# Kernel tuning notes

Hardware: AMD Instinct MI355X
Metric: run time of the kernel (lower is better)

## Reference

```python
import jax, jax.numpy as jnp
import numpy as np


def setup_inputs() -> dict:
    key = jax.random.key(0)
    k1, k2 = jax.random.split(key)
    inputs = jax.random.normal(k1, (64, 32, 32, 64), dtype=jnp.float32)
    # codebook param: (embedding_dim=64, n_embedding=1024), variance-scaling uniform fan_in
    fan_in = 64
    limit = float(np.sqrt(3.0 / fan_in))
    embeddings = jax.random.uniform(k2, (64, 1024), dtype=jnp.float32,
                                    minval=-limit, maxval=limit)
    return {"inputs": inputs, "embeddings": embeddings}


def reference(inputs, embeddings):
    commitment_cost = 0.25
    D, K = embeddings.shape  # (embedding_dim, n_embedding)
    flat = inputs.reshape(-1, D)  # [N, D]
    distances = (jnp.sum(jnp.square(flat), 1, keepdims=True)
                 - 2.0 * jnp.matmul(flat, embeddings)
                 + jnp.sum(jnp.square(embeddings), 0, keepdims=True))
    encoding_indices_flat = jnp.argmax(-distances, 1)  # [N]
    encodings = jax.nn.one_hot(encoding_indices_flat, K, dtype=distances.dtype)  # [N, K]
    encoding_indices = encoding_indices_flat.reshape(inputs.shape[:-1])  # [B,H,W]
    quantized = embeddings.T[encoding_indices]  # gather -> [B,H,W,D]

    e_latent_loss = jnp.mean(jnp.square(jax.lax.stop_gradient(quantized) - inputs))
    q_latent_loss = jnp.mean(jnp.square(quantized - jax.lax.stop_gradient(inputs)))
    loss = q_latent_loss + commitment_cost * e_latent_loss

    # straight-through estimator
    quantized_st = inputs + jax.lax.stop_gradient(quantized - inputs)

    avg_probs = jnp.mean(encodings, 0)
    perplexity = jnp.exp(-jnp.sum(avg_probs * jnp.log(avg_probs + 1e-10)))
    return (quantized_st, loss, perplexity, encodings, encoding_indices, distances)
```

## Files before the change

### kernel.cpp

```cpp
#include <hip/hip_runtime.h>
#include <math.h>

#define NROWS   65536
#define DIMS    64
#define KCODES  1024
#define RPB     16
#define NTHR    256

static constexpr size_t QST_OFF  = 0;
static constexpr size_t LOSS_OFF = 4194304;
static constexpr size_t PERP_OFF = 4194305;
static constexpr size_t ENC_OFF  = 4194306;
static constexpr size_t IDX_OFF  = 71303170;
static constexpr size_t DIST_OFF = 71368706;

__global__ void enorm_kernel(const float* __restrict__ emb, float* __restrict__ enorm) {
    #pragma clang fp contract(off)
    int k = blockIdx.x * blockDim.x + threadIdx.x;
    float s = 0.f;
    for (int d = 0; d < DIMS; ++d) {
        float e  = emb[(size_t)d * KCODES + k];
        float sq = e * e;
        s = s + sq;
    }
    enorm[k] = s;
}

__global__ __launch_bounds__(NTHR) void vq_main(
    const float* __restrict__ x, const float* __restrict__ emb,
    const float* __restrict__ enorm, float* __restrict__ out,
    float* __restrict__ counts, float* __restrict__ sqsum)
{
    #pragma clang fp contract(off)
    __shared__ float xs[RPB * DIMS];
    __shared__ float xn[RPB];
    __shared__ float wbv[RPB * 4]; __shared__ int wbi[RPB * 4];
    __shared__ int   winner[RPB];

    const int tid  = threadIdx.x;
    const int lane = tid & 63;
    const int wv   = tid >> 6;
    const size_t n0 = (size_t)blockIdx.x * RPB;

    ((float4*)xs)[tid] = ((const float4*)(x + n0 * DIMS))[tid];
    __syncthreads();

    if (tid < RPB) {
        const float* xr = xs + tid * DIMS;
        float rr[8];
        #pragma unroll
        for (int j = 0; j < 8; ++j) { float v = xr[j]; rr[j] = v * v; }
        #pragma unroll
        for (int i = 8; i < 64; i += 8) {
            #pragma unroll
            for (int j = 0; j < 8; ++j) { float v = xr[i + j]; float sq = v * v; rr[j] = rr[j] + sq; }
        }
        xn[tid] = ((rr[0] + rr[1]) + (rr[2] + rr[3])) + ((rr[4] + rr[5]) + (rr[6] + rr[7]));
    }
    __syncthreads();

    const float e0 = enorm[tid], e1 = enorm[tid + 256],
                e2 = enorm[tid + 512], e3 = enorm[tid + 768];

    float acc[RPB][4];
    #pragma unroll
    for (int r = 0; r < RPB; ++r) { acc[r][0] = acc[r][1] = acc[r][2] = acc[r][3] = 0.f; }

    const float* ep = emb + tid;
    #pragma unroll 2
    for (int d = 0; d < DIMS; ++d) {
        float g0 = ep[0], g1 = ep[256], g2 = ep[512], g3 = ep[768];
        ep += KCODES;
        #pragma unroll
        for (int r = 0; r < RPB; ++r) {
            float xv = xs[r * DIMS + d];
            acc[r][0] = fmaf(xv, g0, acc[r][0]);
            acc[r][1] = fmaf(xv, g1, acc[r][1]);
            acc[r][2] = fmaf(xv, g2, acc[r][2]);
            acc[r][3] = fmaf(xv, g3, acc[r][3]);
        }
    }

    float* distb = out + DIST_OFF;
    float* encb  = out + ENC_OFF;

    #pragma unroll
    for (int r = 0; r < RPB; ++r) {
        const float xnr = xn[r];
        float m0 = 2.0f * acc[r][0]; float t0 = xnr - m0; float d0 = t0 + e0;
        float m1 = 2.0f * acc[r][1]; float t1 = xnr - m1; float d1 = t1 + e1;
        float m2 = 2.0f * acc[r][2]; float t2 = xnr - m2; float d2 = t2 + e2;
        float m3 = 2.0f * acc[r][3]; float t3 = xnr - m3; float d3 = t3 + e3;

        float* dr = distb + (n0 + r) * (size_t)KCODES;
        dr[tid] = d0; dr[tid + 256] = d1; dr[tid + 512] = d2; dr[tid + 768] = d3;
        float* er = encb + (n0 + r) * (size_t)KCODES;
        er[tid] = 0.f; er[tid + 256] = 0.f; er[tid + 512] = 0.f; er[tid + 768] = 0.f;

        float bv = d0; int bi = tid;
        if (d1 < bv) { bv = d1; bi = tid + 256; }
        if (d2 < bv) { bv = d2; bi = tid + 512; }
        if (d3 < bv) { bv = d3; bi = tid + 768; }

        #pragma unroll
        for (int m = 1; m < 64; m <<= 1) {
            float ov = __shfl_xor(bv, m); int oi = __shfl_xor(bi, m);
            if (ov < bv || (ov == bv && oi < bi)) { bv = ov; bi = oi; }
        }
        if (lane == 0) { wbv[r * 4 + wv] = bv; wbi[r * 4 + wv] = bi; }
    }

    __syncthreads();

    if (tid < RPB) {
        float bv = wbv[tid * 4]; int bi = wbi[tid * 4];
        for (int w = 1; w < 4; ++w) {
            float ov = wbv[tid * 4 + w]; int oi = wbi[tid * 4 + w];
            if (ov < bv || (ov == bv && oi < bi)) { bv = ov; bi = oi; }
        }
        winner[tid] = bi;
        out[IDX_OFF + n0 + tid] = (float)bi;
        atomicAdd(&counts[bi], 1.0f);
        encb[(n0 + tid) * (size_t)KCODES + bi] = 1.0f;
    }
    __syncthreads();

    {
        int r  = tid >> 4;
        int dd = (tid & 15) * 4;
        int kk = winner[r];
        float4 q;
        q.x = emb[(size_t)(dd + 0) * KCODES + kk];
        q.y = emb[(size_t)(dd + 1) * KCODES + kk];
        q.z = emb[(size_t)(dd + 2) * KCODES + kk];
        q.w = emb[(size_t)(dd + 3) * KCODES + kk];
        *(float4*)(out + QST_OFF + (n0 + r) * DIMS + dd) = q;
        float f0 = q.x - xs[r*DIMS+dd+0], f1 = q.y - xs[r*DIMS+dd+1];
        float f2 = q.z - xs[r*DIMS+dd+2], f3 = q.w - xs[r*DIMS+dd+3];
        float ls = f0*f0 + f1*f1 + f2*f2 + f3*f3;
        #pragma unroll
        for (int m = 1; m < 64; m <<= 1) ls += __shfl_xor(ls, m);
        if (lane == 0) atomicAdd(sqsum, ls);
    }
}

__global__ void vq_final(const float* __restrict__ counts, const float* __restrict__ sqsum,
                         float* __restrict__ out) {
    __shared__ float part[16];
    int tid = threadIdx.x;
    float p = counts[tid] * (1.0f / 65536.0f);
    float t = p * logf(p + 1e-10f);
    #pragma unroll
    for (int m = 1; m < 64; m <<= 1) t += __shfl_xor(t, m);
    if ((tid & 63) == 0) part[tid >> 6] = t;
    __syncthreads();
    if (tid == 0) {
        float s = 0.f;
        #pragma unroll
        for (int i = 0; i < 16; ++i) s += part[i];
        out[LOSS_OFF] = 1.25f * sqsum[0] * (1.0f / 4194304.0f);
        out[PERP_OFF] = expf(-s);
    }
}

extern "C" void kernel_launch(void* const* d_in, const int* in_sizes, int n_in,
                              void* d_out, int out_size, void* d_ws, size_t ws_size,
                              hipStream_t stream) {
    const float* x   = (const float*)d_in[0];
    const float* emb = (const float*)d_in[1];
    float* out    = (float*)d_out;
    float* enorm  = (float*)d_ws;
    float* counts = enorm + KCODES;
    float* sqsum  = counts + KCODES;

    hipMemsetAsync(counts, 0, (KCODES + 1) * sizeof(float), stream);
    enorm_kernel<<<KCODES / NTHR, NTHR, 0, stream>>>(emb, enorm);
    vq_main<<<NROWS / RPB, NTHR, 0, stream>>>(x, emb, enorm, out, counts, sqsum);
    vq_final<<<1, KCODES, 0, stream>>>(counts, sqsum, out);
}
```

Measured before the change: 286.5 us.

## Retile distance GEMM to 8x8 register blocks with vectorized loads

Restructures the distance matmul so each thread computes an 8-row by 8-code tile: two 128-thread groups each take 8 rows, and each thread covers 4 contiguous codes in each half of the codebook. It uses float4 loads of x from shared memory and float4 codebook loads, which raises FMA-to-load reuse. Distance and one-hot stores become float2 vectors, and the cross-wave argmin reduction shrinks from 4 partials to 2. It also moves the perplexity/loss final reduction to double precision, a numerical-accuracy change rather than a speed change. The larger register tile and the float4 loads with a 4-element stride per thread change coalescing patterns.

```diff
diff --git a/kernel.cpp b/kernel.cpp
--- a/kernel.cpp
+++ b/kernel.cpp
@@ -32,14 +32,16 @@
     float* __restrict__ counts, float* __restrict__ sqsum)
 {
     #pragma clang fp contract(off)
-    __shared__ float xs[RPB * DIMS];
+    __shared__ __align__(16) float xs[RPB * DIMS];
     __shared__ float xn[RPB];
-    __shared__ float wbv[RPB * 4]; __shared__ int wbi[RPB * 4];
+    __shared__ float wbv[RPB * 2]; __shared__ int wbi[RPB * 2];
     __shared__ int   winner[RPB];
 
     const int tid  = threadIdx.x;
     const int lane = tid & 63;
     const int wv   = tid >> 6;
+    const int gid  = tid >> 7;
+    const int l7   = tid & 127;
     const size_t n0 = (size_t)blockIdx.x * RPB;
 
     ((float4*)xs)[tid] = ((const float4*)(x + n0 * DIMS))[tid];
@@ -59,65 +61,91 @@
     }
     __syncthreads();
 
-    const float e0 = enorm[tid], e1 = enorm[tid + 256],
-                e2 = enorm[tid + 512], e3 = enorm[tid + 768];
-
-    float acc[RPB][4];
+    float acc[8][8];
     #pragma unroll
-    for (int r = 0; r < RPB; ++r) { acc[r][0] = acc[r][1] = acc[r][2] = acc[r][3] = 0.f; }
-
-    const float* ep = emb + tid;
-    #pragma unroll 2
-    for (int d = 0; d < DIMS; ++d) {
-        float g0 = ep[0], g1 = ep[256], g2 = ep[512], g3 = ep[768];
-        ep += KCODES;
-        #pragma unroll
-        for (int r = 0; r < RPB; ++r) {
-            float xv = xs[r * DIMS + d];
-            acc[r][0] = fmaf(xv, g0, acc[r][0]);
-            acc[r][1] = fmaf(xv, g1, acc[r][1]);
-            acc[r][2] = fmaf(xv, g2, acc[r][2]);
-            acc[r][3] = fmaf(xv, g3, acc[r][3]);
+    for (int r = 0; r < 8; ++r)
+        #pragma unroll
+        for (int j = 0; j < 8; ++j) acc[r][j] = 0.f;
+
+    const float* embk = emb + l7 * 4;
+    const float* xbase = xs + gid * 8 * DIMS;
+    #pragma unroll 1
+    for (int d0 = 0; d0 < DIMS; d0 += 4) {
+        float4 xv[8];
+        #pragma unroll
+        for (int r = 0; r < 8; ++r) xv[r] = *(const float4*)(xbase + r * DIMS + d0);
+        #pragma unroll
+        for (int c = 0; c < 2; ++c) {
+            const float* ep = embk + d0 * KCODES + c * 512;
+            float4 g0 = *(const float4*)(ep);
+            float4 g1 = *(const float4*)(ep + KCODES);
+            float4 g2 = *(const float4*)(ep + 2 * KCODES);
+            float4 g3 = *(const float4*)(ep + 3 * KCODES);
+            #pragma unroll
+            for (int r = 0; r < 8; ++r) {
+                float4 xv4 = xv[r];
+                float a0 = acc[r][c*4+0], a1 = acc[r][c*4+1], a2 = acc[r][c*4+2], a3 = acc[r][c*4+3];
+                a0 = fmaf(xv4.x, g0.x, a0); a0 = fmaf(xv4.y, g1.x, a0); a0 = fmaf(xv4.z, g2.x, a0); a0 = fmaf(xv4.w, g3.x, a0);
+                a1 = fmaf(xv4.x, g0.y, a1); a1 = fmaf(xv4.y, g1.y, a1); a1 = fmaf(xv4.z, g2.y, a1); a1 = fmaf(xv4.w, g3.y, a1);
+                a2 = fmaf(xv4.x, g0.z, a2); a2 = fmaf(xv4.y, g1.z, a2); a2 = fmaf(xv4.z, g2.z, a2); a2 = fmaf(xv4.w, g3.z, a2);
+                a3 = fmaf(xv4.x, g0.w, a3); a3 = fmaf(xv4.y, g1.w, a3); a3 = fmaf(xv4.z, g2.w, a3); a3 = fmaf(xv4.w, g3.w, a3);
+                acc[r][c*4+0] = a0; acc[r][c*4+1] = a1; acc[r][c*4+2] = a2; acc[r][c*4+3] = a3;
+            }
         }
     }
 
+    const float4 e0 = *(const float4*)(enorm + l7 * 4);
+    const float4 e1 = *(const float4*)(enorm + 512 + l7 * 4);
     float* distb = out + DIST_OFF;
     float* encb  = out + ENC_OFF;
 
     #pragma unroll
-    for (int r = 0; r < RPB; ++r) {
-        const float xnr = xn[r];
-        float m0 = 2.0f * acc[r][0]; float t0 = xnr - m0; float d0 = t0 + e0;
-        float m1 = 2.0f * acc[r][1]; float t1 = xnr - m1; float d1 = t1 + e1;
-        float m2 = 2.0f * acc[r][2]; float t2 = xnr - m2; float d2 = t2 + e2;
-        float m3 = 2.0f * acc[r][3]; float t3 = xnr - m3; float d3 = t3 + e3;
-
-        float* dr = distb + (n0 + r) * (size_t)KCODES;
-        dr[tid] = d0; dr[tid + 256] = d1; dr[tid + 512] = d2; dr[tid + 768] = d3;
-        float* er = encb + (n0 + r) * (size_t)KCODES;
-        er[tid] = 0.f; er[tid + 256] = 0.f; er[tid + 512] = 0.f; er[tid + 768] = 0.f;
-
-        float bv = d0; int bi = tid;
-        if (d1 < bv) { bv = d1; bi = tid + 256; }
-        if (d2 < bv) { bv = d2; bi = tid + 512; }
-        if (d3 < bv) { bv = d3; bi = tid + 768; }
+    for (int r = 0; r < 8; ++r) {
+        const int row = gid * 8 + r;
+        const float xnr = xn[row];
+        float dv[8];
+        { float m = 2.0f * acc[r][0]; float t = xnr - m; dv[0] = t + e0.x; }
+        { float m = 2.0f * acc[r][1]; float t = xnr - m; dv[1] = t + e0.y; }
+        { float m = 2.0f * acc[r][2]; float t = xnr - m; dv[2] = t + e0.z; }
+        { float m = 2.0f * acc[r][3]; float t = xnr - m; dv[3] = t + e0.w; }
+        { float m = 2.0f * acc[r][4]; float t = xnr - m; dv[4] = t + e1.x; }
+        { float m = 2.0f * acc[r][5]; float t = xnr - m; dv[5] = t + e1.y; }
+        { float m = 2.0f * acc[r][6]; float t = xnr - m; dv[6] = t + e1.z; }
+        { float m = 2.0f * acc[r][7]; float t = xnr - m; dv[7] = t + e1.w; }
+
+        float* dr = distb + (n0 + row) * (size_t)KCODES + l7 * 4;
+        *(float2*)(dr)       = make_float2(dv[0], dv[1]);
+        *(float2*)(dr + 2)   = make_float2(dv[2], dv[3]);
+        *(float2*)(dr + 512) = make_float2(dv[4], dv[5]);
+        *(float2*)(dr + 514) = make_float2(dv[6], dv[7]);
+        float* er = encb + (n0 + row) * (size_t)KCODES + l7 * 4;
+        const float2 z2 = make_float2(0.f, 0.f);
+        *(float2*)(er) = z2; *(float2*)(er + 2) = z2;
+        *(float2*)(er + 512) = z2; *(float2*)(er + 514) = z2;
+
+        float bv = dv[0]; int bi = l7 * 4;
+        if (dv[1] < bv) { bv = dv[1]; bi = l7 * 4 + 1; }
+        if (dv[2] < bv) { bv = dv[2]; bi = l7 * 4 + 2; }
+        if (dv[3] < bv) { bv = dv[3]; bi = l7 * 4 + 3; }
+        if (dv[4] < bv) { bv = dv[4]; bi = 512 + l7 * 4; }
+        if (dv[5] < bv) { bv = dv[5]; bi = 512 + l7 * 4 + 1; }
+        if (dv[6] < bv) { bv = dv[6]; bi = 512 + l7 * 4 + 2; }
+        if (dv[7] < bv) { bv = dv[7]; bi = 512 + l7 * 4 + 3; }
 
         #pragma unroll
         for (int m = 1; m < 64; m <<= 1) {
             float ov = __shfl_xor(bv, m); int oi = __shfl_xor(bi, m);
             if (ov < bv || (ov == bv && oi < bi)) { bv = ov; bi = oi; }
         }
-        if (lane == 0) { wbv[r * 4 + wv] = bv; wbi[r * 4 + wv] = bi; }
+        if (lane == 0) { wbv[row * 2 + (wv & 1)] = bv; wbi[row * 2 + (wv & 1)] = bi; }
     }
 
     __syncthreads();
 
     if (tid < RPB) {
-        float bv = wbv[tid * 4]; int bi = wbi[tid * 4];
-        for (int w = 1; w < 4; ++w) {
-            float ov = wbv[tid * 4 + w]; int oi = wbi[tid * 4 + w];
-            if (ov < bv || (ov == bv && oi < bi)) { bv = ov; bi = oi; }
-        }
+        float bv = wbv[tid * 2]; int bi = wbi[tid * 2];
+        float ov = wbv[tid * 2 + 1]; int oi = wbi[tid * 2 + 1];
+        if (ov < bv || (ov == bv && oi < bi)) { bv = ov; bi = oi; }
         winner[tid] = bi;
         out[IDX_OFF + n0 + tid] = (float)bi;
         atomicAdd(&counts[bi], 1.0f);
@@ -146,20 +174,20 @@
 
 __global__ void vq_final(const float* __restrict__ counts, const float* __restrict__ sqsum,
                          float* __restrict__ out) {
-    __shared__ float part[16];
+    __shared__ double part[16];
     int tid = threadIdx.x;
-    float p = counts[tid] * (1.0f / 65536.0f);
-    float t = p * logf(p + 1e-10f);
+    double p = (double)counts[tid] * (1.0 / 65536.0);
+    double t = p * log(p + 1e-10);
     #pragma unroll
     for (int m = 1; m < 64; m <<= 1) t += __shfl_xor(t, m);
     if ((tid & 63) == 0) part[tid >> 6] = t;
     __syncthreads();
     if (tid == 0) {
-        float s = 0.f;
+        double s = 0.0;
         #pragma unroll
         for (int i = 0; i < 16; ++i) s += part[i];
-        out[LOSS_OFF] = 1.25f * sqsum[0] * (1.0f / 4194304.0f);
-        out[PERP_OFF] = expf(-s);
+        out[LOSS_OFF] = (float)(1.25 * (double)sqsum[0] * (1.0 / 4194304.0));
+        out[PERP_OFF] = (float)exp(-s);
     }
 }
 
```

New measurement: 270.6 us. 1.06x faster.

## Tile distance GEMM into 128x128 blocks with global atomicMin argmin and separate finish kernel

Applied to the files above, without the earlier changes.

Replaces the per-16-row kernel, which re-read the whole codebook from global memory for every block, with a 128-row by 128-code tiled kernel. It stages transposed x and codebook slices in shared memory and gives each thread a 4x8 register tile. The argmin is combined across code tiles with a packed 64-bit atomicMin on an order-preserving key, and a new finish kernel does the gather, loss, indices and one-hot writes. This cuts redundant codebook traffic and raises arithmetic intensity. The cost is an extra kernel launch, an extra memset for the winners buffer, and vectorized float4 stores for the large distance and encoding outputs. The perplexity reduction also moves to double precision.

```diff
diff --git a/kernel.cpp b/kernel.cpp
--- a/kernel.cpp
+++ b/kernel.cpp
@@ -4,8 +4,6 @@
 #define NROWS   65536
 #define DIMS    64
 #define KCODES  1024
-#define RPB     16
-#define NTHR    256
 
 static constexpr size_t QST_OFF  = 0;
 static constexpr size_t LOSS_OFF = 4194304;
@@ -13,6 +11,8 @@
 static constexpr size_t ENC_OFF  = 4194306;
 static constexpr size_t IDX_OFF  = 71303170;
 static constexpr size_t DIST_OFF = 71368706;
+
+#define XSTRIDE 132
 
 __global__ void enorm_kernel(const float* __restrict__ emb, float* __restrict__ enorm) {
     #pragma clang fp contract(off)
@@ -26,140 +26,190 @@
     enorm[k] = s;
 }
 
-__global__ __launch_bounds__(NTHR) void vq_main(
+__global__ __launch_bounds__(512, 4) void vq_dist(
     const float* __restrict__ x, const float* __restrict__ emb,
     const float* __restrict__ enorm, float* __restrict__ out,
+    unsigned long long* __restrict__ winners)
+{
+    #pragma clang fp contract(off)
+    __shared__ __align__(16) float xs_t[32 * XSTRIDE];
+    __shared__ __align__(16) float es_t[32 * XSTRIDE];
+    __shared__ float xnl[128];
+
+    const int tid = threadIdx.x;
+    const int tc  = tid & 15;
+    const int tr  = tid >> 4;
+    const int kt  = blockIdx.x & 7;
+    const int br  = blockIdx.x >> 3;
+    const size_t n0 = (size_t)br * 128;
+
+    const float* xg = x + n0 * DIMS;
+    const float* eg = emb + kt * 128;
+
+    float acc[4][8];
+    #pragma unroll
+    for (int j = 0; j < 4; ++j)
+        #pragma unroll
+        for (int jj = 0; jj < 8; ++jj) acc[j][jj] = 0.f;
+
+    float rr[8];
+
+    for (int h = 0; h < 2; ++h) {
+        __syncthreads();
+        #pragma unroll
+        for (int i = 0; i < 2; ++i) {
+            int c = tid + 512 * i;
+            int row = c >> 3, dq = c & 7;
+            float4 v = *(const float4*)(xg + (size_t)row * DIMS + h * 32 + dq * 4);
+            xs_t[(dq * 4 + 0) * XSTRIDE + row] = v.x;
+            xs_t[(dq * 4 + 1) * XSTRIDE + row] = v.y;
+            xs_t[(dq * 4 + 2) * XSTRIDE + row] = v.z;
+            xs_t[(dq * 4 + 3) * XSTRIDE + row] = v.w;
+        }
+        #pragma unroll
+        for (int i = 0; i < 2; ++i) {
+            int c = tid + 512 * i;
+            int d2 = c >> 5, kq = c & 31;
+            float4 v = *(const float4*)(eg + (size_t)(h * 32 + d2) * KCODES + kq * 4);
+            es_t[d2 * XSTRIDE + kq * 4 + 0] = v.x;
+            es_t[d2 * XSTRIDE + kq * 4 + 1] = v.y;
+            es_t[d2 * XSTRIDE + kq * 4 + 2] = v.z;
+            es_t[d2 * XSTRIDE + kq * 4 + 3] = v.w;
+        }
+        __syncthreads();
+
+        if (tid < 128) {
+            if (h == 0) {
+                #pragma unroll
+                for (int j = 0; j < 8; ++j) { float v = xs_t[j * XSTRIDE + tid]; rr[j] = v * v; }
+                for (int i = 8; i < 32; i += 8)
+                    #pragma unroll
+                    for (int j = 0; j < 8; ++j) { float v = xs_t[(i + j) * XSTRIDE + tid]; float sq = v * v; rr[j] = rr[j] + sq; }
+            } else {
+                for (int i = 0; i < 32; i += 8)
+                    #pragma unroll
+                    for (int j = 0; j < 8; ++j) { float v = xs_t[(i + j) * XSTRIDE + tid]; float sq = v * v; rr[j] = rr[j] + sq; }
+                xnl[tid] = ((rr[0] + rr[1]) + (rr[2] + rr[3])) + ((rr[4] + rr[5]) + (rr[6] + rr[7]));
+            }
+        }
+
+        #pragma unroll 4
+        for (int d2 = 0; d2 < 32; ++d2) {
+            float4 xr = *(const float4*)&xs_t[d2 * XSTRIDE + tr * 4];
+            float4 ea = *(const float4*)&es_t[d2 * XSTRIDE + tc * 4];
+            float4 eb = *(const float4*)&es_t[d2 * XSTRIDE + 64 + tc * 4];
+            float xv[4] = {xr.x, xr.y, xr.z, xr.w};
+            #pragma unroll
+            for (int j = 0; j < 4; ++j) {
+                acc[j][0] = fmaf(xv[j], ea.x, acc[j][0]);
+                acc[j][1] = fmaf(xv[j], ea.y, acc[j][1]);
+                acc[j][2] = fmaf(xv[j], ea.z, acc[j][2]);
+                acc[j][3] = fmaf(xv[j], ea.w, acc[j][3]);
+                acc[j][4] = fmaf(xv[j], eb.x, acc[j][4]);
+                acc[j][5] = fmaf(xv[j], eb.y, acc[j][5]);
+                acc[j][6] = fmaf(xv[j], eb.z, acc[j][6]);
+                acc[j][7] = fmaf(xv[j], eb.w, acc[j][7]);
+            }
+        }
+    }
+    __syncthreads();
+
+    const float4 en0 = *(const float4*)(enorm + kt * 128 + tc * 4);
+    const float4 en1 = *(const float4*)(enorm + kt * 128 + 64 + tc * 4);
+    const float4 z4 = make_float4(0.f, 0.f, 0.f, 0.f);
+
+    #pragma unroll
+    for (int j = 0; j < 4; ++j) {
+        const int row = tr * 4 + j;
+        const float xnr = xnl[row];
+        float4 da, db;
+        { float m = 2.0f * acc[j][0]; float t = xnr - m; da.x = t + en0.x; }
+        { float m = 2.0f * acc[j][1]; float t = xnr - m; da.y = t + en0.y; }
+        { float m = 2.0f * acc[j][2]; float t = xnr - m; da.z = t + en0.z; }
+        { float m = 2.0f * acc[j][3]; float t = xnr - m; da.w = t + en0.w; }
+        { float m = 2.0f * acc[j][4]; float t = xnr - m; db.x = t + en1.x; }
+        { float m = 2.0f * acc[j][5]; float t = xnr - m; db.y = t + en1.y; }
+        { float m = 2.0f * acc[j][6]; float t = xnr - m; db.z = t + en1.z; }
+        { float m = 2.0f * acc[j][7]; float t = xnr - m; db.w = t + en1.w; }
+
+        const size_t rowg = n0 + row;
+        float* dr = out + DIST_OFF + rowg * (size_t)KCODES + kt * 128 + tc * 4;
+        *(float4*)dr = da; *(float4*)(dr + 64) = db;
+        float* er = out + ENC_OFF + rowg * (size_t)KCODES + kt * 128 + tc * 4;
+        *(float4*)er = z4; *(float4*)(er + 64) = z4;
+
+        float bv = da.x; int kloc = tc * 4;
+        if (da.y < bv) { bv = da.y; kloc = tc * 4 + 1; }
+        if (da.z < bv) { bv = da.z; kloc = tc * 4 + 2; }
+        if (da.w < bv) { bv = da.w; kloc = tc * 4 + 3; }
+        if (db.x < bv) { bv = db.x; kloc = 64 + tc * 4; }
+        if (db.y < bv) { bv = db.y; kloc = 64 + tc * 4 + 1; }
+        if (db.z < bv) { bv = db.z; kloc = 64 + tc * 4 + 2; }
+        if (db.w < bv) { bv = db.w; kloc = 64 + tc * 4 + 3; }
+
+        int ib = __float_as_int(bv);
+        unsigned mk = (unsigned)ib ^ ((unsigned)(ib >> 31) | 0x80000000u);
+        unsigned long long key = ((unsigned long long)mk << 32) | (unsigned)(kt * 128 + kloc);
+
+        #pragma unroll
+        for (int m = 1; m < 16; m <<= 1) {
+            unsigned long long ok = __shfl_xor(key, m);
+            if (ok < key) key = ok;
+        }
+        if (tc == 0) atomicMin(&winners[rowg], key);
+    }
+}
+
+__global__ __launch_bounds__(256) void vq_finish(
+    const float* __restrict__ x, const float* __restrict__ emb,
+    const unsigned long long* __restrict__ winners, float* __restrict__ out,
     float* __restrict__ counts, float* __restrict__ sqsum)
 {
-    #pragma clang fp contract(off)
-    __shared__ float xs[RPB * DIMS];
-    __shared__ float xn[RPB];
-    __shared__ float wbv[RPB * 4]; __shared__ int wbi[RPB * 4];
-    __shared__ int   winner[RPB];
-
-    const int tid  = threadIdx.x;
-    const int lane = tid & 63;
-    const int wv   = tid >> 6;
-    const size_t n0 = (size_t)blockIdx.x * RPB;
-
-    ((float4*)xs)[tid] = ((const float4*)(x + n0 * DIMS))[tid];
+    __shared__ float bsum[4];
+    const int tid = threadIdx.x;
+    const size_t row = (size_t)blockIdx.x * 16 + (tid >> 4);
+    const int q = tid & 15;
+    const int k = (int)(winners[row] & 1023u);
+
+    float4 e4;
+    e4.x = emb[(size_t)(q * 4 + 0) * KCODES + k];
+    e4.y = emb[(size_t)(q * 4 + 1) * KCODES + k];
+    e4.z = emb[(size_t)(q * 4 + 2) * KCODES + k];
+    e4.w = emb[(size_t)(q * 4 + 3) * KCODES + k];
+    float4 x4 = *(const float4*)(x + row * DIMS + q * 4);
+    *(float4*)(out + QST_OFF + row * DIMS + q * 4) = e4;
+
+    float f0 = e4.x - x4.x, f1 = e4.y - x4.y, f2 = e4.z - x4.z, f3 = e4.w - x4.w;
+    float ls = f0 * f0 + f1 * f1 + f2 * f2 + f3 * f3;
+    #pragma unroll
+    for (int m = 1; m < 64; m <<= 1) ls += __shfl_xor(ls, m);
+    if ((tid & 63) == 0) bsum[tid >> 6] = ls;
+
+    if (q == 0) {
+        out[IDX_OFF + row] = (float)k;
+        atomicAdd(&counts[k], 1.0f);
+        out[ENC_OFF + row * (size_t)KCODES + k] = 1.0f;
+    }
     __syncthreads();
-
-    if (tid < RPB) {
-        const float* xr = xs + tid * DIMS;
-        float rr[8];
-        #pragma unroll
-        for (int j = 0; j < 8; ++j) { float v = xr[j]; rr[j] = v * v; }
-        #pragma unroll
-        for (int i = 8; i < 64; i += 8) {
-            #pragma unroll
-            for (int j = 0; j < 8; ++j) { float v = xr[i + j]; float sq = v * v; rr[j] = rr[j] + sq; }
-        }
-        xn[tid] = ((rr[0] + rr[1]) + (rr[2] + rr[3])) + ((rr[4] + rr[5]) + (rr[6] + rr[7]));
-    }
-    __syncthreads();
-
-    const float e0 = enorm[tid], e1 = enorm[tid + 256],
-                e2 = enorm[tid + 512], e3 = enorm[tid + 768];
-
-    float acc[RPB][4];
-    #pragma unroll
-    for (int r = 0; r < RPB; ++r) { acc[r][0] = acc[r][1] = acc[r][2] = acc[r][3] = 0.f; }
-
-    const float* ep = emb + tid;
-    #pragma unroll 2
-    for (int d = 0; d < DIMS; ++d) {
-        float g0 = ep[0], g1 = ep[256], g2 = ep[512], g3 = ep[768];
-        ep += KCODES;
-        #pragma unroll
-        for (int r = 0; r < RPB; ++r) {
-            float xv = xs[r * DIMS + d];
-            acc[r][0] = fmaf(xv, g0, acc[r][0]);
-            acc[r][1] = fmaf(xv, g1, acc[r][1]);
-            acc[r][2] = fmaf(xv, g2, acc[r][2]);
-            acc[r][3] = fmaf(xv, g3, acc[r][3]);
-        }
-    }
-
-    float* distb = out + DIST_OFF;
-    float* encb  = out + ENC_OFF;
-
-    #pragma unroll
-    for (int r = 0; r < RPB; ++r) {
-        const float xnr = xn[r];
-        float m0 = 2.0f * acc[r][0]; float t0 = xnr - m0; float d0 = t0 + e0;
-        float m1 = 2.0f * acc[r][1]; float t1 = xnr - m1; float d1 = t1 + e1;
-        float m2 = 2.0f * acc[r][2]; float t2 = xnr - m2; float d2 = t2 + e2;
-        float m3 = 2.0f * acc[r][3]; float t3 = xnr - m3; float d3 = t3 + e3;
-
-        float* dr = distb + (n0 + r) * (size_t)KCODES;
-        dr[tid] = d0; dr[tid + 256] = d1; dr[tid + 512] = d2; dr[tid + 768] = d3;
-        float* er = encb + (n0 + r) * (size_t)KCODES;
-        er[tid] = 0.f; er[tid + 256] = 0.f; er[tid + 512] = 0.f; er[tid + 768] = 0.f;
-
-        float bv = d0; int bi = tid;
-        if (d1 < bv) { bv = d1; bi = tid + 256; }
-        if (d2 < bv) { bv = d2; bi = tid + 512; }
-        if (d3 < bv) { bv = d3; bi = tid + 768; }
-
-        #pragma unroll
-        for (int m = 1; m < 64; m <<= 1) {
-            float ov = __shfl_xor(bv, m); int oi = __shfl_xor(bi, m);
-            if (ov < bv || (ov == bv && oi < bi)) { bv = ov; bi = oi; }
-        }
-        if (lane == 0) { wbv[r * 4 + wv] = bv; wbi[r * 4 + wv] = bi; }
-    }
-
-    __syncthreads();
-
-    if (tid < RPB) {
-        float bv = wbv[tid * 4]; int bi = wbi[tid * 4];
-        for (int w = 1; w < 4; ++w) {
-            float ov = wbv[tid * 4 + w]; int oi = wbi[tid * 4 + w];
-            if (ov < bv || (ov == bv && oi < bi)) { bv = ov; bi = oi; }
-        }
-        winner[tid] = bi;
-        out[IDX_OFF + n0 + tid] = (float)bi;
-        atomicAdd(&counts[bi], 1.0f);
-        encb[(n0 + tid) * (size_t)KCODES + bi] = 1.0f;
-    }
-    __syncthreads();
-
-    {
-        int r  = tid >> 4;
-        int dd = (tid & 15) * 4;
-        int kk = winner[r];
-        float4 q;
-        q.x = emb[(size_t)(dd + 0) * KCODES + kk];
-        q.y = emb[(size_t)(dd + 1) * KCODES + kk];
-        q.z = emb[(size_t)(dd + 2) * KCODES + kk];
-        q.w = emb[(size_t)(dd + 3) * KCODES + kk];
-        *(float4*)(out + QST_OFF + (n0 + r) * DIMS + dd) = q;
-        float f0 = q.x - xs[r*DIMS+dd+0], f1 = q.y - xs[r*DIMS+dd+1];
-        float f2 = q.z - xs[r*DIMS+dd+2], f3 = q.w - xs[r*DIMS+dd+3];
-        float ls = f0*f0 + f1*f1 + f2*f2 + f3*f3;
-        #pragma unroll
-        for (int m = 1; m < 64; m <<= 1) ls += __shfl_xor(ls, m);
-        if (lane == 0) atomicAdd(sqsum, ls);
-    }
+    if (tid == 0) atomicAdd(sqsum, (bsum[0] + bsum[1]) + (bsum[2] + bsum[3]));
 }
 
 __global__ void vq_final(const float* __restrict__ counts, const float* __restrict__ sqsum,
                          float* __restrict__ out) {
-    __shared__ float part[16];
+    __shared__ double part[16];
     int tid = threadIdx.x;
-    float p = counts[tid] * (1.0f / 65536.0f);
-    float t = p * logf(p + 1e-10f);
+    double p = (double)counts[tid] * (1.0 / 65536.0);
+    double t = p * log(p + 1e-10);
     #pragma unroll
     for (int m = 1; m < 64; m <<= 1) t += __shfl_xor(t, m);
     if ((tid & 63) == 0) part[tid >> 6] = t;
     __syncthreads();
     if (tid == 0) {
-        float s = 0.f;
+        double s = 0.0;
         #pragma unroll
         for (int i = 0; i < 16; ++i) s += part[i];
-        out[LOSS_OFF] = 1.25f * sqsum[0] * (1.0f / 4194304.0f);
-        out[PERP_OFF] = expf(-s);
+        out[LOSS_OFF] = (float)(1.25 * (double)sqsum[0] * (1.0 / 4194304.0));
+        out[PERP_OFF] = (float)exp(-s);
     }
 }
 
@@ -168,13 +218,16 @@
                               hipStream_t stream) {
     const float* x   = (const float*)d_in[0];
     const float* emb = (const float*)d_in[1];
-    float* out    = (float*)d_out;
+    float* out = (float*)d_out;
     float* enorm  = (float*)d_ws;
     float* counts = enorm + KCODES;
     float* sqsum  = counts + KCODES;
+    unsigned long long* winners = (unsigned long long*)((float*)d_ws + 4096);
 
     hipMemsetAsync(counts, 0, (KCODES + 1) * sizeof(float), stream);
-    enorm_kernel<<<KCODES / NTHR, NTHR, 0, stream>>>(emb, enorm);
-    vq_main<<<NROWS / RPB, NTHR, 0, stream>>>(x, emb, enorm, out, counts, sqsum);
+    hipMemsetAsync(winners, 0xFF, NROWS * sizeof(unsigned long long), stream);
+    enorm_kernel<<<KCODES / 256, 256, 0, stream>>>(emb, enorm);
+    vq_dist<<<(NROWS / 128) * (KCODES / 128), 512, 0, stream>>>(x, emb, enorm, out, winners);
+    vq_finish<<<NROWS / 16, 256, 0, stream>>>(x, emb, winners, out, counts, sqsum);
     vq_final<<<1, KCODES, 0, stream>>>(counts, sqsum, out);
 }
```

Result: faster. 264.8 us (-7.6%).
